# Optimization experiments

Hardware: AMD Instinct MI355X
Metric: run time of the kernel (lower is better)

Reference implementation:

```python
import jax, jax.numpy as jnp
import numpy as np
import math

N, B, E = 1024, 1, 1024
H = 16
D = E // H
S = 128  # num_samples per row

def setup_inputs() -> dict:
    key = jax.random.key(0)
    ks = jax.random.split(key, 12)
    w = lambda k: jax.random.normal(k, (E, E), jnp.float32) * 0.02
    inp = {
        'query': jax.random.normal(ks[0], (N, B, E), jnp.float32),
        'key':   jax.random.normal(ks[1], (N, B, E), jnp.float32),
        'value': jax.random.normal(ks[2], (N, B, E), jnp.float32),
        'Wq': w(ks[3]), 'bq': jnp.zeros((E,), jnp.float32),
        'Wk': w(ks[4]), 'bk': jnp.zeros((E,), jnp.float32),
        'Wv': w(ks[5]), 'bv': jnp.zeros((E,), jnp.float32),
        'Wo': w(ks[6]), 'bo': jnp.zeros((E,), jnp.float32),
        # per-row sampled column indices, already offset+clamped to [0, N)
        'samples': jax.random.randint(ks[7], (N, S), 0, N, jnp.int32),
    }
    return inp

def reference(query, key, value, Wq, bq, Wk, bk, Wv, bv, Wo, bo, samples):
    n = query.shape[0]
    # projections (torch Linear: x @ W.T + b), split heads -> [B*H, n, D]
    q = (query @ Wq.T + bq).reshape(n, B * H, D).transpose(1, 0, 2)
    k = (key   @ Wk.T + bk).reshape(n, B * H, D).transpose(1, 0, 2)
    v = (value @ Wv.T + bv).reshape(n, B * H, D).transpose(1, 0, 2)
    # emulate per-row unique(): sort, mask duplicates (first occurrence kept)
    cols = jnp.sort(samples, axis=1)                              # [n, S]
    dup = jnp.concatenate([jnp.zeros((n, 1), bool), cols[:, 1:] == cols[:, :-1]], axis=1)
    kg = k[:, cols]                                               # [BH, n, S, D]
    scores = jnp.einsum('hid,hisd->his', q, kg) / jnp.float32(math.sqrt(n))
    scores = jnp.where(dup[None], jnp.float32(-1e30), scores)
    w = jax.nn.softmax(scores, axis=-1)                           # [BH, n, S]
    vg = v[:, cols]                                               # [BH, n, S, D]
    o = jnp.einsum('his,hisd->hid', w, vg)                        # [BH, n, D]
    o = o.transpose(1, 0, 2).reshape(n, B, E)
    return o @ Wo.T + bo
```

## Files before the change

### kernel.cpp

```cpp
#include <hip/hip_runtime.h>
#include <hip/hip_bf16.h>

#define NTOK 1024
#define EMB  1024
#define NH   16
#define HD   64
#define NS   128

typedef unsigned short u16;
typedef unsigned int uint;
typedef __attribute__((ext_vector_type(8))) unsigned short ushort8v;
typedef __attribute__((ext_vector_type(8))) _Float16 half8v;
typedef __attribute__((ext_vector_type(4))) float f32x4;

__device__ __forceinline__ u16 f2h_bits(float f) {
  union { _Float16 h; u16 u; } x; x.h = (_Float16)f; return x.u;
}

__device__ __forceinline__ void gload16(const u16* g, u16* l) {
  __builtin_amdgcn_global_load_lds(
      (const __attribute__((address_space(1))) uint*)g,
      (__attribute__((address_space(3))) uint*)l, 16, 0, 0);
}

__global__ __launch_bounds__(256) void cvt_mask(const float* __restrict__ S0,
                                                const float* __restrict__ S1,
                                                const float* __restrict__ S2,
                                                const float* __restrict__ S3,
                                                const float* __restrict__ S4,
                                                const float* __restrict__ S5,
                                                const float* __restrict__ S6,
                                                const int* __restrict__ samples,
                                                u16* __restrict__ D,
                                                uint* __restrict__ maskg) {
  const int z = blockIdx.y;
  const int t = threadIdx.x;
  if (z == 7) {
    __shared__ uint m[32];
    const int i = blockIdx.x;
    if (t < 32) m[t] = 0u;
    __syncthreads();
    if (t < NS) {
      const int c = samples[(size_t)i * NS + t];
      atomicOr(&m[c >> 5], 1u << (c & 31));
    }
    __syncthreads();
    if (t < 32) maskg[(size_t)i * 32 + t] = m[t];
    return;
  }
  const float* S;
  switch (z) {
    case 0: S = S0; break;
    case 1: S = S1; break;
    case 2: S = S2; break;
    case 3: S = S3; break;
    case 4: S = S4; break;
    case 5: S = S5; break;
    default: S = S6; break;
  }
  const int idx = blockIdx.x * 256 + t;
  const float4 f = ((const float4*)S)[idx];
  ushort4 p;
  p.x = f2h_bits(f.x); p.y = f2h_bits(f.y);
  p.z = f2h_bits(f.z); p.w = f2h_bits(f.w);
  ((ushort4*)(D + ((size_t)z << 20)))[idx] = p;
}

template<bool OUT_F16>
__global__ __launch_bounds__(256) void gemm3(const u16* __restrict__ Ab,
                                             const u16* __restrict__ Bb,
                                             const float* __restrict__ b0,
                                             const float* __restrict__ b1,
                                             const float* __restrict__ b2,
                                             void* __restrict__ Cp) {
  __shared__ u16 buf[2][2][64 * 32];

  const int t = threadIdx.x;
  const int lane = t & 63;
  const int w = t >> 6;
  const int wr = w >> 1, wc = w & 1;
  const int m0 = blockIdx.y * 64;
  const int n0 = blockIdx.x * 64;
  const int z = blockIdx.z;

  const u16* Az = Ab + ((size_t)z << 20);
  const u16* Bz = Bb + ((size_t)z << 20);
  const float* bsel = (z == 0) ? b0 : ((z == 1) ? b1 : b2);

  const int r_abs = w * 16 + (lane >> 2);
  const int schunk = (lane & 3) ^ ((r_abs >> 1) & 3);
  const u16* gA = Az + (size_t)(m0 + r_abs) * 1024 + schunk * 8;
  const u16* gB = Bz + (size_t)(n0 + r_abs) * 1024 + schunk * 8;
  u16* ldsA[2] = { &buf[0][0][(w * 16) * 32], &buf[1][0][(w * 16) * 32] };
  u16* ldsB[2] = { &buf[0][1][(w * 16) * 32], &buf[1][1][(w * 16) * 32] };

  const int fr = lane & 15;
  const int fq = lane >> 4;
  int offA[2], offB[2];
#pragma unroll
  for (int m = 0; m < 2; m++) {
    const int R = wr * 32 + m * 16 + fr;
    offA[m] = R * 32 + (fq ^ ((R >> 1) & 3)) * 8;
  }
#pragma unroll
  for (int n = 0; n < 2; n++) {
    const int R = wc * 32 + n * 16 + fr;
    offB[n] = R * 32 + (fq ^ ((R >> 1) & 3)) * 8;
  }

  f32x4 acc[2][2];
#pragma unroll
  for (int m = 0; m < 2; m++)
#pragma unroll
    for (int n = 0; n < 2; n++) acc[m][n] = (f32x4){0.f, 0.f, 0.f, 0.f};

  gload16(gA, ldsA[0]);
  gload16(gB, ldsB[0]);

  for (int kt = 0; kt < 32; kt++) {
    const int db = kt & 1;
    if (kt < 31) {
      const int k1 = (kt + 1) * 32;
      gload16(gA + k1, ldsA[db ^ 1]);
      gload16(gB + k1, ldsB[db ^ 1]);
      asm volatile("s_waitcnt vmcnt(2)" ::: "memory");
    } else {
      asm volatile("s_waitcnt vmcnt(0)" ::: "memory");
    }
    __builtin_amdgcn_s_barrier();
    __builtin_amdgcn_sched_barrier(0);

    const u16* cA = &buf[db][0][0];
    const u16* cB = &buf[db][1][0];
    half8v a0 = *(const half8v*)&cA[offA[0]];
    half8v a1 = *(const half8v*)&cA[offA[1]];
    half8v bv0 = *(const half8v*)&cB[offB[0]];
    half8v bv1 = *(const half8v*)&cB[offB[1]];
    acc[0][0] = __builtin_amdgcn_mfma_f32_16x16x32_f16(a0, bv0, acc[0][0], 0, 0, 0);
    acc[0][1] = __builtin_amdgcn_mfma_f32_16x16x32_f16(a0, bv1, acc[0][1], 0, 0, 0);
    acc[1][0] = __builtin_amdgcn_mfma_f32_16x16x32_f16(a1, bv0, acc[1][0], 0, 0, 0);
    acc[1][1] = __builtin_amdgcn_mfma_f32_16x16x32_f16(a1, bv1, acc[1][1], 0, 0, 0);

    asm volatile("s_waitcnt lgkmcnt(0)" ::: "memory");
    __builtin_amdgcn_s_barrier();
    __builtin_amdgcn_sched_barrier(0);
  }

  u16*   Cb = (u16*)Cp   + ((size_t)z << 20);
  float* Cf = (float*)Cp + ((size_t)z << 20);

  if (OUT_F16 && z == 2) {
#pragma unroll
    for (int n = 0; n < 2; n++) {
      const int col = n0 + wc * 32 + n * 16 + fr;
      const float bn = bsel[col];
#pragma unroll
      for (int m = 0; m < 2; m++) {
        const int rbase = m0 + wr * 32 + m * 16 + fq * 4;
        ushort4 pk;
        pk.x = f2h_bits(acc[m][n][0] + bn);
        pk.y = f2h_bits(acc[m][n][1] + bn);
        pk.z = f2h_bits(acc[m][n][2] + bn);
        pk.w = f2h_bits(acc[m][n][3] + bn);
        *(ushort4*)&Cb[(size_t)col * 1024 + rbase] = pk;
      }
    }
    return;
  }

#pragma unroll
  for (int n = 0; n < 2; n++) {
    const int col = n0 + wc * 32 + n * 16 + fr;
    const float bn = bsel[col];
#pragma unroll
    for (int m = 0; m < 2; m++) {
      const int rbase = m0 + wr * 32 + m * 16 + fq * 4;
#pragma unroll
      for (int r = 0; r < 4; r++) {
        const float val = acc[m][n][r] + bn;
        if constexpr (OUT_F16)
          Cb[(size_t)(rbase + r) * 1024 + col] = f2h_bits(val);
        else
          Cf[(size_t)(rbase + r) * 1024 + col] = val;
      }
    }
  }
}

__global__ __launch_bounds__(128) void attn8(const u16* __restrict__ Qh,
                                             const u16* __restrict__ Kh,
                                             const u16* __restrict__ Vtg,
                                             const uint* __restrict__ maskg,
                                             u16* __restrict__ O) {
  const int h  = blockIdx.x;
  const int qt = blockIdx.y;
  const int t  = threadIdx.x;
  const int wid = t >> 6;
  const int lane = t & 63;
  const int fr = lane & 15, fq = lane >> 4;

  __shared__ u16 Kl[2][128 * 64];
  __shared__ u16 Vl[2][64 * 128];
  __shared__ u16 Ps[2][16][136];
  __shared__ uint Ms[32][32];

  {
    const uint4* src = (const uint4*)(maskg + (size_t)qt * 32 * 32);
    uint4* dst = (uint4*)Ms;
    dst[t * 2]     = src[t * 2];
    dst[t * 2 + 1] = src[t * 2 + 1];
  }

  half8v qa0, qa1;
  {
    const u16* qp = Qh + (size_t)(qt * 32 + wid * 16 + fr) * EMB + h * HD + fq * 8;
    qa0 = *(const half8v*)qp;
    qa1 = *(const half8v*)(qp + 32);
  }

  const int kR3  = lane >> 3;
  const int kChO = ((lane & 7) ^ kR3) * 8;
  const u16* kBase = Kh + h * HD + kChO;
  const int vSub = lane >> 4;
  const int vCh  = lane & 15;
  const u16* vBase = Vtg + (size_t)h * HD * NTOK;

  auto STAGE = [&](int kt_, int b_) {
#pragma unroll
    for (int ii = 0; ii < 8; ii++) {
      const int row = wid * 64 + ii * 8 + kR3;
      gload16(kBase + (size_t)(kt_ * 128 + row) * EMB,
              &Kl[b_][(wid * 64 + ii * 8) * 64]);
    }
#pragma unroll
    for (int ii = 0; ii < 8; ii++) {
      const int d = wid * 32 + ii * 4 + vSub;
      const int ch = (vCh ^ (d & 15)) * 8;
      gload16(vBase + (size_t)d * NTOK + kt_ * 128 + ch,
              &Vl[b_][(wid * 32 + ii * 4) * 128]);
    }
  };

  f32x4 oacc[4];
#pragma unroll
  for (int ds = 0; ds < 4; ds++) oacc[ds] = (f32x4){0.f, 0.f, 0.f, 0.f};
  float lsum[4] = {0.f, 0.f, 0.f, 0.f};

  STAGE(0, 0);

  for (int kt = 0; kt < 8; kt++) {
    if (kt < 7) {
      STAGE(kt + 1, (kt + 1) & 1);
      asm volatile("s_waitcnt vmcnt(16)" ::: "memory");
    } else {
      asm volatile("s_waitcnt vmcnt(0)" ::: "memory");
    }
    asm volatile("s_waitcnt lgkmcnt(0)" ::: "memory");
    __builtin_amdgcn_s_barrier();
    __builtin_amdgcn_sched_barrier(0);

    const u16* Kc = &Kl[kt & 1][0];
    const u16* Vc = &Vl[kt & 1][0];

    uint4 mq[4];
#pragma unroll
    for (int r = 0; r < 4; r++)
      mq[r] = *(const uint4*)&Ms[wid * 16 + fq * 4 + r][kt * 4];

#pragma unroll
    for (int jb = 0; jb < 8; jb++) {
      f32x4 s = (f32x4){0.f, 0.f, 0.f, 0.f};
      const int R = jb * 16 + fr;
      const half8v b0 = *(const half8v*)&Kc[R * 64 + (fq ^ (fr & 7)) * 8];
      const half8v b1 = *(const half8v*)&Kc[R * 64 + ((4 + fq) ^ (fr & 7)) * 8];
      s = __builtin_amdgcn_mfma_f32_16x16x32_f16(qa0, b0, s, 0, 0, 0);
      s = __builtin_amdgcn_mfma_f32_16x16x32_f16(qa1, b1, s, 0, 0, 0);
#pragma unroll
      for (int r = 0; r < 4; r++) {
        const uint mw = (jb >> 1) == 0 ? mq[r].x
                      : (jb >> 1) == 1 ? mq[r].y
                      : (jb >> 1) == 2 ? mq[r].z : mq[r].w;
        const float p = ((mw >> ((jb & 1) * 16 + fr)) & 1u)
                            ? __expf(s[r] * 0.03125f) : 0.f;
        lsum[r] += p;
        Ps[wid][fq * 4 + r][jb * 16 + fr] = f2h_bits(p);
      }
    }
    asm volatile("s_waitcnt lgkmcnt(0)" ::: "memory");
    __builtin_amdgcn_sched_barrier(0);

#pragma unroll
    for (int jc = 0; jc < 4; jc++) {
      const half8v pa = *(const half8v*)&Ps[wid][fr][jc * 32 + fq * 8];
#pragma unroll
      for (int ds = 0; ds < 4; ds++) {
        const int d = ds * 16 + fr;
        const half8v vb = *(const half8v*)&Vc[d * 128 + ((jc * 4 + fq) ^ fr) * 8];
        oacc[ds] = __builtin_amdgcn_mfma_f32_16x16x32_f16(pa, vb, oacc[ds], 0, 0, 0);
      }
    }
    __builtin_amdgcn_s_barrier();
  }

#pragma unroll
  for (int r = 0; r < 4; r++) {
    float v = lsum[r];
#pragma unroll
    for (int off = 1; off < 16; off <<= 1) v += __shfl_xor(v, off, 16);
    lsum[r] = v;
  }

#pragma unroll
  for (int ds = 0; ds < 4; ds++) {
#pragma unroll
    for (int r = 0; r < 4; r++) {
      O[(size_t)(qt * 32 + wid * 16 + fq * 4 + r) * EMB + h * HD + ds * 16 + fr] =
          f2h_bits(oacc[ds][r] / lsum[r]);
    }
  }
}

extern "C" void kernel_launch(void* const* d_in, const int* in_sizes, int n_in,
                              void* d_out, int out_size, void* d_ws, size_t ws_size,
                              hipStream_t stream) {
  const float* query = (const float*)d_in[0];
  const float* key   = (const float*)d_in[1];
  const float* value = (const float*)d_in[2];
  const float* Wq    = (const float*)d_in[3];
  const float* bq    = (const float*)d_in[4];
  const float* Wk    = (const float*)d_in[5];
  const float* bk    = (const float*)d_in[6];
  const float* Wv    = (const float*)d_in[7];
  const float* bv    = (const float*)d_in[8];
  const float* Wo    = (const float*)d_in[9];
  const float* bo    = (const float*)d_in[10];
  const int* samples = (const int*)d_in[11];
  float* out = (float*)d_out;

  u16* base = (u16*)d_ws;
  u16* Xh = base;
  u16* Wh = base + ((size_t)3 << 20);
  u16* Qh = base + ((size_t)7 << 20);
  u16* Kh = base + ((size_t)8 << 20);
  u16* Vt = base + ((size_t)9 << 20);
  u16* O  = base + ((size_t)10 << 20);
  uint* maskg = (uint*)(base + ((size_t)11 << 20));

  cvt_mask<<<dim3(1024, 8), 256, 0, stream>>>(
      query, key, value, Wq, Wk, Wv, Wo, samples, Xh, maskg);

  gemm3<true><<<dim3(16, 16, 3), 256, 0, stream>>>(Xh, Wh, bq, bk, bv, Qh);

  attn8<<<dim3(NH, 32), 128, 0, stream>>>(Qh, Kh, Vt, maskg, O);

  gemm3<false><<<dim3(16, 16, 1), 256, 0, stream>>>(O, Wh + ((size_t)3 << 20), bo, bo, bo, out);
}
```

Baseline: 59.37 us.

## Split fused masked attention into separate score and PV kernels via global P buffer

```diff
diff --git a/kernel.cpp b/kernel.cpp
--- a/kernel.cpp
+++ b/kernel.cpp
@@ -187,135 +187,185 @@
   }
 }
 
-__global__ __launch_bounds__(128) void attn8(const u16* __restrict__ Qh,
+__global__ __launch_bounds__(256) void skern(const u16* __restrict__ Qh,
                                              const u16* __restrict__ Kh,
-                                             const u16* __restrict__ Vtg,
                                              const uint* __restrict__ maskg,
-                                             u16* __restrict__ O) {
-  const int h  = blockIdx.x;
-  const int qt = blockIdx.y;
-  const int t  = threadIdx.x;
-  const int wid = t >> 6;
+                                             u16* __restrict__ Pb) {
+  __shared__ u16 sQ[64 * 64];
+  __shared__ u16 sK[64 * 64];
+
+  const int t = threadIdx.x;
   const int lane = t & 63;
+  const int w = t >> 6;
+  const int wr = w >> 1, wc = w & 1;
+  const int m0 = blockIdx.y * 64;
+  const int n0 = blockIdx.x * 64;
+  const int h  = blockIdx.z;
+
+  {
+    const int row0 = t >> 3,        c0 = t & 7;
+    const int row1 = 32 + (t >> 3), c1 = t & 7;
+    const u16* qg = Qh + h * HD;
+    const u16* kg = Kh + h * HD;
+    gload16(qg + (size_t)(m0 + row0) * 1024 + ((c0 ^ (row0 & 7)) * 8), &sQ[(size_t)t * 8]);
+    gload16(qg + (size_t)(m0 + row1) * 1024 + ((c1 ^ (row1 & 7)) * 8), &sQ[(size_t)(256 + t) * 8]);
+    gload16(kg + (size_t)(n0 + row0) * 1024 + ((c0 ^ (row0 & 7)) * 8), &sK[(size_t)t * 8]);
+    gload16(kg + (size_t)(n0 + row1) * 1024 + ((c1 ^ (row1 & 7)) * 8), &sK[(size_t)(256 + t) * 8]);
+  }
+  asm volatile("s_waitcnt vmcnt(0)" ::: "memory");
+  __builtin_amdgcn_s_barrier();
+  __builtin_amdgcn_sched_barrier(0);
+
   const int fr = lane & 15, fq = lane >> 4;
 
-  __shared__ u16 Kl[2][128 * 64];
-  __shared__ u16 Vl[2][64 * 128];
-  __shared__ u16 Ps[2][16][136];
-  __shared__ uint Ms[32][32];
-
-  {
-    const uint4* src = (const uint4*)(maskg + (size_t)qt * 32 * 32);
-    uint4* dst = (uint4*)Ms;
-    dst[t * 2]     = src[t * 2];
-    dst[t * 2 + 1] = src[t * 2 + 1];
-  }
-
-  half8v qa0, qa1;
-  {
-    const u16* qp = Qh + (size_t)(qt * 32 + wid * 16 + fr) * EMB + h * HD + fq * 8;
-    qa0 = *(const half8v*)qp;
-    qa1 = *(const half8v*)(qp + 32);
-  }
-
-  const int kR3  = lane >> 3;
-  const int kChO = ((lane & 7) ^ kR3) * 8;
-  const u16* kBase = Kh + h * HD + kChO;
-  const int vSub = lane >> 4;
-  const int vCh  = lane & 15;
-  const u16* vBase = Vtg + (size_t)h * HD * NTOK;
-
-  auto STAGE = [&](int kt_, int b_) {
-#pragma unroll
-    for (int ii = 0; ii < 8; ii++) {
-      const int row = wid * 64 + ii * 8 + kR3;
-      gload16(kBase + (size_t)(kt_ * 128 + row) * EMB,
-              &Kl[b_][(wid * 64 + ii * 8) * 64]);
-    }
-#pragma unroll
-    for (int ii = 0; ii < 8; ii++) {
-      const int d = wid * 32 + ii * 4 + vSub;
-      const int ch = (vCh ^ (d & 15)) * 8;
-      gload16(vBase + (size_t)d * NTOK + kt_ * 128 + ch,
-              &Vl[b_][(wid * 32 + ii * 4) * 128]);
-    }
-  };
-
-  f32x4 oacc[4];
-#pragma unroll
-  for (int ds = 0; ds < 4; ds++) oacc[ds] = (f32x4){0.f, 0.f, 0.f, 0.f};
-  float lsum[4] = {0.f, 0.f, 0.f, 0.f};
-
-  STAGE(0, 0);
-
-  for (int kt = 0; kt < 8; kt++) {
-    if (kt < 7) {
-      STAGE(kt + 1, (kt + 1) & 1);
-      asm volatile("s_waitcnt vmcnt(16)" ::: "memory");
+  f32x4 acc[2][2];
+#pragma unroll
+  for (int m = 0; m < 2; m++)
+#pragma unroll
+    for (int n = 0; n < 2; n++) acc[m][n] = (f32x4){0.f, 0.f, 0.f, 0.f};
+
+#pragma unroll
+  for (int kk = 0; kk < 2; kk++) {
+    half8v a[2], b[2];
+#pragma unroll
+    for (int m = 0; m < 2; m++) {
+      const int R = wr * 32 + m * 16 + fr;
+      a[m] = *(const half8v*)&sQ[R * 64 + (((kk * 4 + fq) ^ (R & 7)) * 8)];
+    }
+#pragma unroll
+    for (int n = 0; n < 2; n++) {
+      const int R = wc * 32 + n * 16 + fr;
+      b[n] = *(const half8v*)&sK[R * 64 + (((kk * 4 + fq) ^ (R & 7)) * 8)];
+    }
+#pragma unroll
+    for (int m = 0; m < 2; m++)
+#pragma unroll
+      for (int n = 0; n < 2; n++)
+        acc[m][n] = __builtin_amdgcn_mfma_f32_16x16x32_f16(a[m], b[n], acc[m][n], 0, 0, 0);
+  }
+
+  u16* Pz = Pb + ((size_t)h << 20);
+  const int wconst = (n0 >> 5) + wc;
+
+  uint mw[2][4];
+#pragma unroll
+  for (int m = 0; m < 2; m++) {
+    const int rbase = m0 + wr * 32 + m * 16 + fq * 4;
+#pragma unroll
+    for (int r = 0; r < 4; r++)
+      mw[m][r] = maskg[(size_t)(rbase + r) * 32 + wconst];
+  }
+
+#pragma unroll
+  for (int n = 0; n < 2; n++) {
+    const int col = n0 + wc * 32 + n * 16 + fr;
+    const int bit = (n * 16 + fr) & 31;
+#pragma unroll
+    for (int m = 0; m < 2; m++) {
+      const int rbase = m0 + wr * 32 + m * 16 + fq * 4;
+#pragma unroll
+      for (int r = 0; r < 4; r++) {
+        const float p = ((mw[m][r] >> bit) & 1u)
+                            ? __expf(acc[m][n][r] * 0.03125f) : 0.f;
+        Pz[(size_t)(rbase + r) * 1024 + col] = f2h_bits(p);
+      }
+    }
+  }
+}
+
+__global__ __launch_bounds__(256) void pvkern(const u16* __restrict__ Pb,
+                                              const u16* __restrict__ Vt,
+                                              u16* __restrict__ O) {
+  __shared__ u16 buf[2][2][64 * 32];
+
+  const int t = threadIdx.x;
+  const int lane = t & 63;
+  const int w = t >> 6;
+  const int wr = w >> 1, wc = w & 1;
+  const int m0 = blockIdx.x * 64;
+  const int h  = blockIdx.y;
+
+  const u16* Az = Pb + ((size_t)h << 20);
+  const u16* Bz = Vt + (size_t)(h * HD) * 1024;
+
+  const int r_abs = w * 16 + (lane >> 2);
+  const int schunk = (lane & 3) ^ ((r_abs >> 1) & 3);
+  const u16* gA = Az + (size_t)(m0 + r_abs) * 1024 + schunk * 8;
+  const u16* gB = Bz + (size_t)r_abs * 1024 + schunk * 8;
+  u16* ldsA[2] = { &buf[0][0][(w * 16) * 32], &buf[1][0][(w * 16) * 32] };
+  u16* ldsB[2] = { &buf[0][1][(w * 16) * 32], &buf[1][1][(w * 16) * 32] };
+
+  const int fr = lane & 15;
+  const int fq = lane >> 4;
+  int offA[2], offB[2];
+#pragma unroll
+  for (int m = 0; m < 2; m++) {
+    const int R = wr * 32 + m * 16 + fr;
+    offA[m] = R * 32 + (fq ^ ((R >> 1) & 3)) * 8;
+  }
+#pragma unroll
+  for (int n = 0; n < 2; n++) {
+    const int R = wc * 32 + n * 16 + fr;
+    offB[n] = R * 32 + (fq ^ ((R >> 1) & 3)) * 8;
+  }
+
+  f32x4 acc[2][2], accs[2];
+#pragma unroll
+  for (int m = 0; m < 2; m++) {
+    accs[m] = (f32x4){0.f, 0.f, 0.f, 0.f};
+#pragma unroll
+    for (int n = 0; n < 2; n++) acc[m][n] = (f32x4){0.f, 0.f, 0.f, 0.f};
+  }
+
+  half8v ones;
+#pragma unroll
+  for (int i = 0; i < 8; i++) ones[i] = (_Float16)1.0f;
+
+  gload16(gA, ldsA[0]);
+  gload16(gB, ldsB[0]);
+
+  for (int kt = 0; kt < 32; kt++) {
+    const int db = kt & 1;
+    if (kt < 31) {
+      const int k1 = (kt + 1) * 32;
+      gload16(gA + k1, ldsA[db ^ 1]);
+      gload16(gB + k1, ldsB[db ^ 1]);
+      asm volatile("s_waitcnt vmcnt(2)" ::: "memory");
     } else {
       asm volatile("s_waitcnt vmcnt(0)" ::: "memory");
     }
+    __builtin_amdgcn_s_barrier();
+    __builtin_amdgcn_sched_barrier(0);
+
+    const u16* cA = &buf[db][0][0];
+    const u16* cB = &buf[db][1][0];
+    half8v a0 = *(const half8v*)&cA[offA[0]];
+    half8v a1 = *(const half8v*)&cA[offA[1]];
+    half8v bv0 = *(const half8v*)&cB[offB[0]];
+    half8v bv1 = *(const half8v*)&cB[offB[1]];
+    acc[0][0] = __builtin_amdgcn_mfma_f32_16x16x32_f16(a0, bv0, acc[0][0], 0, 0, 0);
+    acc[0][1] = __builtin_amdgcn_mfma_f32_16x16x32_f16(a0, bv1, acc[0][1], 0, 0, 0);
+    acc[1][0] = __builtin_amdgcn_mfma_f32_16x16x32_f16(a1, bv0, acc[1][0], 0, 0, 0);
+    acc[1][1] = __builtin_amdgcn_mfma_f32_16x16x32_f16(a1, bv1, acc[1][1], 0, 0, 0);
+    accs[0]   = __builtin_amdgcn_mfma_f32_16x16x32_f16(a0, ones, accs[0], 0, 0, 0);
+    accs[1]   = __builtin_amdgcn_mfma_f32_16x16x32_f16(a1, ones, accs[1], 0, 0, 0);
+
     asm volatile("s_waitcnt lgkmcnt(0)" ::: "memory");
     __builtin_amdgcn_s_barrier();
     __builtin_amdgcn_sched_barrier(0);
-
-    const u16* Kc = &Kl[kt & 1][0];
-    const u16* Vc = &Vl[kt & 1][0];
-
-    uint4 mq[4];
-#pragma unroll
-    for (int r = 0; r < 4; r++)
-      mq[r] = *(const uint4*)&Ms[wid * 16 + fq * 4 + r][kt * 4];
-
-#pragma unroll
-    for (int jb = 0; jb < 8; jb++) {
-      f32x4 s = (f32x4){0.f, 0.f, 0.f, 0.f};
-      const int R = jb * 16 + fr;
-      const half8v b0 = *(const half8v*)&Kc[R * 64 + (fq ^ (fr & 7)) * 8];
-      const half8v b1 = *(const half8v*)&Kc[R * 64 + ((4 + fq) ^ (fr & 7)) * 8];
-      s = __builtin_amdgcn_mfma_f32_16x16x32_f16(qa0, b0, s, 0, 0, 0);
-      s = __builtin_amdgcn_mfma_f32_16x16x32_f16(qa1, b1, s, 0, 0, 0);
+  }
+
+#pragma unroll
+  for (int n = 0; n < 2; n++) {
+    const int col = wc * 32 + n * 16 + fr;
+#pragma unroll
+    for (int m = 0; m < 2; m++) {
+      const int rbase = m0 + wr * 32 + m * 16 + fq * 4;
 #pragma unroll
       for (int r = 0; r < 4; r++) {
-        const uint mw = (jb >> 1) == 0 ? mq[r].x
-                      : (jb >> 1) == 1 ? mq[r].y
-                      : (jb >> 1) == 2 ? mq[r].z : mq[r].w;
-        const float p = ((mw >> ((jb & 1) * 16 + fr)) & 1u)
-                            ? __expf(s[r] * 0.03125f) : 0.f;
-        lsum[r] += p;
-        Ps[wid][fq * 4 + r][jb * 16 + fr] = f2h_bits(p);
+        O[(size_t)(rbase + r) * 1024 + h * HD + col] =
+            f2h_bits(acc[m][n][r] / accs[m][r]);
       }
-    }
-    asm volatile("s_waitcnt lgkmcnt(0)" ::: "memory");
-    __builtin_amdgcn_sched_barrier(0);
-
-#pragma unroll
-    for (int jc = 0; jc < 4; jc++) {
-      const half8v pa = *(const half8v*)&Ps[wid][fr][jc * 32 + fq * 8];
-#pragma unroll
-      for (int ds = 0; ds < 4; ds++) {
-        const int d = ds * 16 + fr;
-        const half8v vb = *(const half8v*)&Vc[d * 128 + ((jc * 4 + fq) ^ fr) * 8];
-        oacc[ds] = __builtin_amdgcn_mfma_f32_16x16x32_f16(pa, vb, oacc[ds], 0, 0, 0);
-      }
-    }
-    __builtin_amdgcn_s_barrier();
-  }
-
-#pragma unroll
-  for (int r = 0; r < 4; r++) {
-    float v = lsum[r];
-#pragma unroll
-    for (int off = 1; off < 16; off <<= 1) v += __shfl_xor(v, off, 16);
-    lsum[r] = v;
-  }
-
-#pragma unroll
-  for (int ds = 0; ds < 4; ds++) {
-#pragma unroll
-    for (int r = 0; r < 4; r++) {
-      O[(size_t)(qt * 32 + wid * 16 + fq * 4 + r) * EMB + h * HD + ds * 16 + fr] =
-          f2h_bits(oacc[ds][r] / lsum[r]);
     }
   }
 }
@@ -345,13 +395,16 @@
   u16* Vt = base + ((size_t)9 << 20);
   u16* O  = base + ((size_t)10 << 20);
   uint* maskg = (uint*)(base + ((size_t)11 << 20));
+  u16* Pb = base + ((size_t)12 << 20);
 
   cvt_mask<<<dim3(1024, 8), 256, 0, stream>>>(
       query, key, value, Wq, Wk, Wv, Wo, samples, Xh, maskg);
 
   gemm3<true><<<dim3(16, 16, 3), 256, 0, stream>>>(Xh, Wh, bq, bk, bv, Qh);
 
-  attn8<<<dim3(NH, 32), 128, 0, stream>>>(Qh, Kh, Vt, maskg, O);
+  skern<<<dim3(16, 16, 16), 256, 0, stream>>>(Qh, Kh, maskg, Pb);
+
+  pvkern<<<dim3(16, 16), 256, 0, stream>>>(Pb, Vt, O);
 
   gemm3<false><<<dim3(16, 16, 1), 256, 0, stream>>>(O, Wh + ((size_t)3 << 20), bo, bo, bo, out);
 }
```

New measurement: 66.34 us. 1.12x slower.
